# Performance work log

Measured on AMD Instinct MI355X. Metric: run time of the kernel, lower is better.

Reference implementation:

```python
import jax, jax.numpy as jnp
import numpy as np

N_NODES = 50000
N_EDGES = 800000
D = 128
H = 8
HD = D // H
N_NTYPES = 3
N_ETYPES = 5
LN_EPS = 1e-5


def setup_inputs() -> dict:
    key = jax.random.key(0)
    ks = jax.random.split(key, 16)
    inp = {
        "x": jax.random.normal(ks[0], (N_NODES, D), dtype=jnp.float32),
        "edge_index": jax.random.randint(ks[1], (2, N_EDGES), 0, N_NODES),
        "edge_type": jax.random.randint(ks[2], (N_EDGES,), 0, N_ETYPES),
        "node_type": jax.random.randint(ks[3], (N_NODES,), 0, N_NTYPES),
        # per-(node_type, head) QKV projections, per-(edge_type, head) K transform
        "W_Q": jax.random.normal(ks[4], (N_NTYPES, H, HD, HD), dtype=jnp.float32) * 0.02,
        "W_K": jax.random.normal(ks[5], (N_NTYPES, H, HD, HD), dtype=jnp.float32) * 0.02,
        "W_V": jax.random.normal(ks[6], (N_NTYPES, H, HD, HD), dtype=jnp.float32) * 0.02,
        "W_edge": jax.random.normal(ks[7], (N_ETYPES, H, HD, HD), dtype=jnp.float32) * 0.02,
        "mu": jnp.ones((H, N_ETYPES), dtype=jnp.float32),
        "W_out": jax.random.normal(ks[8], (D, D), dtype=jnp.float32) * 0.02,
        "b_out": jnp.zeros((D,), dtype=jnp.float32),
        "ln1_g": jnp.ones((D,), dtype=jnp.float32),
        "ln1_b": jnp.zeros((D,), dtype=jnp.float32),
        "W1": jax.random.normal(ks[9], (D, 4 * D), dtype=jnp.float32) * 0.02,
        "b1": jnp.zeros((4 * D,), dtype=jnp.float32),
        "W2": jax.random.normal(ks[10], (4 * D, D), dtype=jnp.float32) * 0.02,
        "b2": jnp.zeros((D,), dtype=jnp.float32),
        "ln2_g": jnp.ones((D,), dtype=jnp.float32),
        "ln2_b": jnp.zeros((D,), dtype=jnp.float32),
    }
    return inp


def _layer_norm(y, g, b):
    m = y.mean(-1, keepdims=True)
    v = ((y - m) ** 2).mean(-1, keepdims=True)
    return (y - m) * jax.lax.rsqrt(v + LN_EPS) * g + b


def reference(x, edge_index, edge_type, node_type,
              W_Q, W_K, W_V, W_edge, mu,
              W_out, b_out, ln1_g, ln1_b, W1, b1, W2, b2, ln2_g, ln2_b):
    N = x.shape[0]
    xh = x.reshape(N, H, HD)  # heads vectorized (concat of per-head slices)

    # type-specific QKV: small fixed loop over node types, masked select
    Q = jnp.zeros_like(xh)
    K = jnp.zeros_like(xh)
    V = jnp.zeros_like(xh)
    for t in range(N_NTYPES):
        m = (node_type == t)[:, None, None]
        Q = jnp.where(m, jnp.einsum('nhd,hdf->nhf', xh, W_Q[t]), Q)
        K = jnp.where(m, jnp.einsum('nhd,hdf->nhf', xh, W_K[t]), K)
        V = jnp.where(m, jnp.einsum('nhd,hdf->nhf', xh, W_V[t]), V)

    src, dst = edge_index[0], edge_index[1]
    q_dst = Q[dst]   # [E,H,HD]
    k_src = K[src]   # [E,H,HD]

    # edge-type-specific K transform
    kt = jnp.zeros_like(k_src)
    for et in range(N_ETYPES):
        m = (edge_type == et)[:, None, None]
        kt = jnp.where(m, jnp.einsum('ehd,hdf->ehf', k_src, W_edge[et]), kt)

    scores = (q_dst * kt).sum(-1) / jnp.sqrt(jnp.float32(HD))  # [E,H]
    scores = scores * mu[:, edge_type].T                       # mu per edge type, per head

    # sparse softmax over incoming edges of each dst node, per head
    smax = jax.ops.segment_max(scores, dst, num_segments=N)
    ex = jnp.exp(scores - smax[dst])
    den = jax.ops.segment_sum(ex, dst, num_segments=N)
    w = ex / (den[dst] + 1e-10)                                 # [E,H]

    agg = jax.ops.segment_sum(V[src] * w[..., None], dst, num_segments=N)  # [N,H,HD]
    mh = agg.reshape(N, D) @ W_out + b_out  # dropout is identity in eval

    h = _layer_norm(x + mh, ln1_g, ln1_b)
    ffn = jax.nn.gelu(h @ W1 + b1, approximate=False) @ W2 + b2
    return _layer_norm(h + ffn, ln2_g, ln2_b)
```

## Files before the change

kernel.cpp:

```cpp
#include <hip/hip_runtime.h>
#include <hip/hip_bf16.h>

#define N_NODESC 50000
#define N_EDGESC 800000
#define DD 128
#define HH 8
#define HDIM 16
#define N_NT 3
#define N_ET 5
#define NPB 196
#define NEB 400
#define NFB 512
#define WPB 912

#define KV8_OFF    ((size_t)0)
#define QT8_OFF    ((size_t)12800000)
#define AGG_OFF    ((size_t)57600000)
#define WOUTT_OFF  ((size_t)83200000)
#define W1T_OFF    ((size_t)83232768)
#define W2T_OFF    ((size_t)83363840)
#define WHPF_OFF   ((size_t)83494912)
#define EDATA_OFF  ((size_t)84183040)
#define ROWS_OFF   ((size_t)87383040)
#define ORIG_OFF   ((size_t)87583104)
#define DEG_OFF    ((size_t)87783104)
#define TOFS_OFF   ((size_t)87983104)
#define BH_OFF     ((size_t)87983168)
#define BB_OFF     ((size_t)87985536)
#define TMP_OFF    ((size_t)87988928)
#define RLOC_OFF   ((size_t)91188928)
#define CSUM_OFF   ((size_t)91389056)

using short8 = __attribute__((ext_vector_type(8))) short;
using f32x4  = __attribute__((ext_vector_type(4))) float;
using f32x2  = __attribute__((ext_vector_type(2))) float;

__device__ __forceinline__ ushort f2b(float f) {
    __hip_bfloat16 h = __float2bfloat16(f);
    return *(ushort*)&h;
}
__device__ __forceinline__ float b2f(ushort u) {
    __hip_bfloat16 h = *(__hip_bfloat16*)&u;
    return __bfloat162float(h);
}
__device__ __forceinline__ f32x2 pk0(unsigned int w) {
    return __builtin_amdgcn_cvt_pk_f32_fp8((int)w, false);
}
__device__ __forceinline__ f32x2 pk1(unsigned int w) {
    return __builtin_amdgcn_cvt_pk_f32_fp8((int)w, true);
}
__device__ __forceinline__ float gelu_f(float v) {
    const float x = v * 0.70710678118654752f;
    const float ax = fabsf(x);
    const float d = fmaf(0.3275911f, ax, 1.0f);
    float t;
    asm("v_rcp_f32 %0, %1" : "=v"(t) : "v"(d));
    float p = fmaf(1.061405429f, t, -1.453152027f);
    p = fmaf(p, t, 1.421413741f);
    p = fmaf(p, t, -0.284496736f);
    p = fmaf(p, t, 0.254829592f);
    p = p * t;
    const float e = __expf(-ax * ax);
    const float er = 1.0f - p * e;
    const float erfx = (x < 0.f) ? -er : er;
    return 0.5f * v * (1.0f + erfx);
}
__device__ __forceinline__ void ebar() {
    __builtin_amdgcn_sched_barrier(0);
    asm volatile("s_waitcnt lgkmcnt(0)" ::: "memory");
    __builtin_amdgcn_sched_barrier(0);
    __builtin_amdgcn_s_barrier();
    __builtin_amdgcn_sched_barrier(0);
}

__global__ __launch_bounds__(256) void prep_a(
    const float* __restrict__ Wout, const float* __restrict__ W1, const float* __restrict__ W2,
    const float* __restrict__ WQ, const float* __restrict__ Wk, const float* __restrict__ Wv,
    const float* __restrict__ We, const float* __restrict__ mu,
    ushort* __restrict__ Woutt, ushort* __restrict__ W1t, ushort* __restrict__ W2t,
    ushort* __restrict__ Whpf,
    const int* __restrict__ ntype, int* __restrict__ bh,
    const int* __restrict__ dst, int* __restrict__ deg, unsigned int* __restrict__ tmp)
{
    const int b = blockIdx.x, tid = threadIdx.x;
    if (b < WPB) {
        const int gid = b * 256 + tid;
        if (gid < 16384) {
            const int nn = gid >> 7, k = gid & 127;
            Woutt[gid] = f2b(Wout[k * 128 + nn]);
        } else if (gid < 81920) {
            const int i = gid - 16384;
            const int nn = i >> 7, k = i & 127;
            W1t[i] = f2b(W1[k * 512 + nn]);
        } else if (gid < 147456) {
            const int i = gid - 81920;
            const int nn = i >> 9, k = i & 511;
            W2t[i] = f2b(W2[k * 128 + nn]);
        } else {
            const int idx = gid - 147456;
            const int t = idx / 28672;
            const int r = idx % 28672;
            const int i = r & 7;
            const int l = (r >> 3) & 63;
            const int f = r >> 9;
            const int j = f % 14, p = f / 14;
            const int c = j * 16 + (l & 15);
            const int k = ((l >> 4) << 3) + i;
            const int hi = (c >= 112) ? 1 : 0;
            const int h = 2 * p + hi;
            float v = 0.f;
            if ((k >> 4) == hi) {
                const int kp = k & 15;
                const int cl = c - hi * 112;
                if (cl < 16) {
                    v = 4.f * Wk[((t * HH + h) * HDIM + kp) * HDIM + cl];
                } else if (cl < 32) {
                    v = 4.f * Wv[((t * HH + h) * HDIM + kp) * HDIM + (cl - 16)];
                } else {
                    const int et = (cl - 32) >> 4, jj = (cl - 32) & 15;
                    const float* wq = WQ + ((t * HH + h) * HDIM + kp) * HDIM;
                    const float* we = We + ((et * HH + h) * HDIM + jj) * HDIM;
                    float s = 0.f;
#pragma unroll
                    for (int ff = 0; ff < 16; ff++) s = fmaf(wq[ff], we[ff], s);
                    v = 64.f * mu[h * N_ET + et] * s;
                }
            }
            Whpf[idx] = f2b(v);
        }
    } else if (b < WPB + NPB) {
        const int bc = b - WPB;
        const int wave = tid >> 6, lane = tid & 63;
        const int n = bc * 256 + tid;
        const int t = (n < N_NODESC) ? ntype[n] : -1;
        const unsigned long long m0 = __ballot(t == 0);
        const unsigned long long m1 = __ballot(t == 1);
        const unsigned long long m2 = __ballot(t == 2);
        __shared__ int wcnt[4][3];
        if (lane == 0) {
            wcnt[wave][0] = (int)__popcll(m0);
            wcnt[wave][1] = (int)__popcll(m1);
            wcnt[wave][2] = (int)__popcll(m2);
        }
        __syncthreads();
        if (tid < 3)
            bh[tid * NPB + bc] = wcnt[0][tid] + wcnt[1][tid] + wcnt[2][tid] + wcnt[3][tid];
    } else {
        for (int e = (b - WPB - NPB) * 256 + tid; e < N_EDGESC; e += NEB * 256) {
            const int nd = dst[e];
            const unsigned int p = (unsigned int)atomicAdd(&deg[nd], 1);
            tmp[e] = (p << 16) | (unsigned int)nd;
        }
    }
}

__global__ __launch_bounds__(256) void prep_b(
    const int* __restrict__ bh, const int* __restrict__ deg,
    int* __restrict__ bb, int* __restrict__ tofs,
    int* __restrict__ rloc, int* __restrict__ csum)
{
    __shared__ int part[256];
    const int tid = threadIdx.x;
    if (blockIdx.x == 0) {
        const int base3 = tid * 3;
        int e0 = (base3 + 0 < 588) ? bh[base3 + 0] : 0;
        int e1 = (base3 + 1 < 588) ? bh[base3 + 1] : 0;
        int e2 = (base3 + 2 < 588) ? bh[base3 + 2] : 0;
        const int l0 = e0, l1 = e0 + e1, l2 = l1 + e2;
        part[tid] = l2;
        __syncthreads();
        for (int off = 1; off < 256; off <<= 1) {
            const int u = (tid >= off) ? part[tid - off] : 0;
            __syncthreads();
            part[tid] += u;
            __syncthreads();
        }
        const int tb = part[tid] - l2;
        if (base3 + 0 < 588) bb[base3 + 0] = tb;
        if (base3 + 1 < 588) bb[base3 + 1] = tb + l0;
        if (base3 + 2 < 588) bb[base3 + 2] = tb + l1;
        __syncthreads();
        if (tid == 0) {
            tofs[0] = 0;
            tofs[1] = bb[NPB];
            tofs[2] = bb[2 * NPB];
            tofs[3] = N_NODESC;
        }
    } else {
        const int c = blockIdx.x - 1;
        const int n = c * 256 + tid;
        const int vdeg = (n < N_NODESC) ? deg[n] : 0;
        part[tid] = vdeg;
        __syncthreads();
        for (int off = 1; off < 256; off <<= 1) {
            const int u = (tid >= off) ? part[tid - off] : 0;
            __syncthreads();
            part[tid] += u;
            __syncthreads();
        }
        if (n <= N_NODESC) rloc[n] = part[tid] - vdeg;
        if (tid == 255) csum[c] = part[255];
    }
}

__global__ __launch_bounds__(256) void prep_c(
    const int* __restrict__ ntype,
    const int* __restrict__ src, const int* __restrict__ etype,
    const int* __restrict__ bb, const int* __restrict__ rloc, const int* __restrict__ csum,
    const unsigned int* __restrict__ tmp,
    int* __restrict__ origof, int* __restrict__ rows,
    int* __restrict__ edata)
{
    const int b = blockIdx.x, tid = threadIdx.x;
    __shared__ int cb[256];
    {
        const int v = (tid < NPB) ? csum[tid] : 0;
        cb[tid] = v;
        __syncthreads();
        for (int off = 1; off < 256; off <<= 1) {
            const int u = (tid >= off) ? cb[tid - off] : 0;
            __syncthreads();
            cb[tid] += u;
            __syncthreads();
        }
        const int incl = cb[tid];
        __syncthreads();
        cb[tid] = incl - v;
        __syncthreads();
    }

    if (b < NPB) {
        const int wave = tid >> 6, lane = tid & 63;
        const int n = b * 256 + tid;
        const int t = (n < N_NODESC) ? ntype[n] : -1;
        const unsigned long long m0 = __ballot(t == 0);
        const unsigned long long m1 = __ballot(t == 1);
        const unsigned long long m2 = __ballot(t == 2);
        __shared__ int wcnt[4][3];
        if (lane == 0) {
            wcnt[wave][0] = (int)__popcll(m0);
            wcnt[wave][1] = (int)__popcll(m1);
            wcnt[wave][2] = (int)__popcll(m2);
        }
        __syncthreads();
        if (n < N_NODESC) {
            int basew = 0;
#pragma unroll
            for (int w = 0; w < 4; w++) if (w < wave) basew += wcnt[w][t];
            const unsigned long long mt = (t == 0) ? m0 : (t == 1) ? m1 : m2;
            const unsigned long long mlt = ((unsigned long long)1 << lane) - 1;
            const int p = bb[t * NPB + b] + basew + (int)__popcll(mt & mlt);
            origof[p] = n;
        }
        if (n <= N_NODESC) rows[n] = cb[b] + rloc[n];
    } else {
        for (int e = (b - NPB) * 256 + tid; e < N_EDGESC; e += NFB * 256) {
            const unsigned int v = tmp[e];
            const int nd = (int)(v & 0xffffu);
            const int p = (int)(v >> 16);
            edata[cb[nd >> 8] + rloc[nd] + p] = src[e] | (etype[e] << 16);
        }
    }
}

#define LDX 132

__global__ __launch_bounds__(256) void proj_gemm(
    const float* __restrict__ x, const ushort* __restrict__ Whpf,
    const int* __restrict__ tofs, const int* __restrict__ origof,
    unsigned char* __restrict__ KV8b, unsigned char* __restrict__ Qt8)
{
    const int t = blockIdx.y;
    const int rs = tofs[t], re = tofs[t + 1];
    const int mBase = rs + blockIdx.x * 64;
    if (mBase >= re) return;

    __shared__ ushort Xs[64 * LDX];
    __shared__ ushort Ws[28672];

    const int tid = threadIdx.x;
    const int lane = tid & 63, wave = tid >> 6;
    const int l15 = lane & 15, rq = (lane >> 4) * 4;

#pragma unroll
    for (int it = 0; it < 4; it++) {
        const int idx = it * 256 + tid;
        const int row = idx >> 4, ch = idx & 15;
        int gm = mBase + row; if (gm >= N_NODESC) gm = N_NODESC - 1;
        const int og = origof[gm];
        const float4 v0 = *(const float4*)(x + (size_t)og * DD + ch * 8);
        const float4 v1 = *(const float4*)(x + (size_t)og * DD + ch * 8 + 4);
        ushort o[8] = {f2b(v0.x), f2b(v0.y), f2b(v0.z), f2b(v0.w),
                       f2b(v1.x), f2b(v1.y), f2b(v1.z), f2b(v1.w)};
        *(uint4*)&Xs[row * LDX + ch * 8] = *(uint4*)o;
    }
    const ushort* Wg = Whpf + (size_t)t * 28672;
#pragma unroll
    for (int it = 0; it < 14; it++) {
        const int idx = it * 256 + tid;
        *(uint4*)&Ws[idx * 8] = *(const uint4*)(Wg + (size_t)idx * 8);
    }
    __syncthreads();

    int ogr[4]; bool vr[4];
#pragma unroll
    for (int r = 0; r < 4; r++) {
        const int gm = mBase + wave * 16 + rq + r;
        vr[r] = (gm < re);
        ogr[r] = vr[r] ? origof[gm] : 0;
    }

    for (int p = 0; p < 4; p++) {
        const short8 af = *(const short8*)&Xs[(wave * 16 + l15) * LDX + p * 32 + (lane >> 4) * 8];
#pragma unroll
        for (int j = 0; j < 14; j++) {
            const short8 bf = *(const short8*)&Ws[((p * 14 + j) * 64 + lane) * 8];
            f32x4 c = __builtin_amdgcn_mfma_f32_16x16x32_bf16(
                af, bf, (f32x4){0.f, 0.f, 0.f, 0.f}, 0, 0, 0);
            const int hi = (j >= 7) ? 1 : 0;
            const int h = 2 * p + hi;
            const int jj = j - hi * 7;
#pragma unroll
            for (int r = 0; r < 4; r++) {
                if (!vr[r]) continue;
                const float v = c[r];
                const unsigned char b8 =
                    (unsigned char)(__builtin_amdgcn_cvt_pk_fp8_f32(v, v, 0, false) & 0xff);
                const size_t og = (size_t)ogr[r];
                if (jj == 0)      KV8b[og * 256 + h * 16 + l15] = b8;
                else if (jj == 1) KV8b[og * 256 + 128 + h * 16 + l15] = b8;
                else              Qt8[og * 640 + (jj - 2) * 128 + h * 16 + l15] = b8;
            }
        }
    }
}

__global__ __launch_bounds__(128) void edgeagg_kernel(
    const int* __restrict__ rowstart, const int* __restrict__ edata,
    const unsigned char* __restrict__ Qt8, const unsigned char* __restrict__ KV8,
    ushort* __restrict__ agg)
{
    const int w = threadIdx.x >> 6;
    const int lane = threadIdx.x & 63;
    const int n = blockIdx.x * 2 + w;
    const int slot = lane >> 3;
    const int h = lane & 7;

    __shared__ uint4 qs8s[2][40];
    if (lane < 40)
        qs8s[w][lane] = ((const uint4*)(Qt8 + (size_t)n * 640))[lane];
    __syncthreads();
    const uint* qbase = (const uint*)&qs8s[w][0];

    const int s0 = rowstart[n], s1 = rowstart[n + 1];
    const float qsc = 1.44269504f / 1024.f;

    float acc[16];
#pragma unroll
    for (int j = 0; j < 16; j++) acc[j] = 0.f;
    float den = 0.f;

    int i = s0 + slot;
    int ed = 0;
    uint4 kw = {0u, 0u, 0u, 0u}, vw = {0u, 0u, 0u, 0u};
    if (i < s1) {
        ed = edata[i];
        const unsigned char* kvp = KV8 + ((size_t)(ed & 0xffff) << 8);
        kw = *(const uint4*)(kvp + (h << 4));
        vw = *(const uint4*)(kvp + 128 + (h << 4));
    }
    while (i < s1) {
        const int in2 = i + 8;
        int edn = 0;
        uint4 kwn = {0u, 0u, 0u, 0u}, vwn = {0u, 0u, 0u, 0u};
        if (in2 < s1) {
            edn = edata[in2];
            const unsigned char* kvpn = KV8 + ((size_t)(edn & 0xffff) << 8);
            kwn = *(const uint4*)(kvpn + (h << 4));
            vwn = *(const uint4*)(kvpn + 128 + (h << 4));
        }

        const int et = ed >> 16;
        const uint4 qw = *(const uint4*)(qbase + (et << 5) + (h << 2));

        const f32x2 q0 = pk0(qw.x), q1 = pk1(qw.x), q2 = pk0(qw.y), q3 = pk1(qw.y);
        const f32x2 q4 = pk0(qw.z), q5 = pk1(qw.z), q6 = pk0(qw.w), q7 = pk1(qw.w);
        const f32x2 k0 = pk0(kw.x), k1 = pk1(kw.x), k2 = pk0(kw.y), k3 = pk1(kw.y);
        const f32x2 k4 = pk0(kw.z), k5 = pk1(kw.z), k6 = pk0(kw.w), k7 = pk1(kw.w);

        float pa = q0.x * k0.x;
        float pb = q0.y * k0.y;
        float pc = q1.x * k1.x;
        float pd = q1.y * k1.y;
        pa = fmaf(q2.x, k2.x, pa); pb = fmaf(q2.y, k2.y, pb);
        pc = fmaf(q3.x, k3.x, pc); pd = fmaf(q3.y, k3.y, pd);
        pa = fmaf(q4.x, k4.x, pa); pb = fmaf(q4.y, k4.y, pb);
        pc = fmaf(q5.x, k5.x, pc); pd = fmaf(q5.y, k5.y, pd);
        pa = fmaf(q6.x, k6.x, pa); pb = fmaf(q6.y, k6.y, pb);
        pc = fmaf(q7.x, k7.x, pc); pd = fmaf(q7.y, k7.y, pd);

        const float ex = exp2f(((pa + pb) + (pc + pd)) * qsc);
        den += ex;

        const f32x2 v0 = pk0(vw.x), v1 = pk1(vw.x), v2 = pk0(vw.y), v3 = pk1(vw.y);
        const f32x2 v4 = pk0(vw.z), v5 = pk1(vw.z), v6 = pk0(vw.w), v7 = pk1(vw.w);
        acc[0]  = fmaf(ex, v0.x, acc[0]);  acc[1]  = fmaf(ex, v0.y, acc[1]);
        acc[2]  = fmaf(ex, v1.x, acc[2]);  acc[3]  = fmaf(ex, v1.y, acc[3]);
        acc[4]  = fmaf(ex, v2.x, acc[4]);  acc[5]  = fmaf(ex, v2.y, acc[5]);
        acc[6]  = fmaf(ex, v3.x, acc[6]);  acc[7]  = fmaf(ex, v3.y, acc[7]);
        acc[8]  = fmaf(ex, v4.x, acc[8]);  acc[9]  = fmaf(ex, v4.y, acc[9]);
        acc[10] = fmaf(ex, v5.x, acc[10]); acc[11] = fmaf(ex, v5.y, acc[11]);
        acc[12] = fmaf(ex, v6.x, acc[12]); acc[13] = fmaf(ex, v6.y, acc[13]);
        acc[14] = fmaf(ex, v7.x, acc[14]); acc[15] = fmaf(ex, v7.y, acc[15]);

        i = in2; ed = edn; kw = kwn; vw = vwn;
    }

    {
        const int b0 = slot & 1, b1 = slot & 2, b2 = slot & 4;
#pragma unroll
        for (int j = 0; j < 8; j++) {
            const float v = b0 ? acc[j] : acc[j + 8];
            const float r = __shfl_xor(v, 8);
            acc[j] = (b0 ? acc[j + 8] : acc[j]) + r;
        }
#pragma unroll
        for (int j = 0; j < 4; j++) {
            const float v = b1 ? acc[j] : acc[j + 4];
            const float r = __shfl_xor(v, 16);
            acc[j] = (b1 ? acc[j + 4] : acc[j]) + r;
        }
#pragma unroll
        for (int j = 0; j < 2; j++) {
            const float v = b2 ? acc[j] : acc[j + 2];
            const float r = __shfl_xor(v, 32);
            acc[j] = (b2 ? acc[j + 2] : acc[j]) + r;
        }
        den += __shfl_xor(den, 8);
        den += __shfl_xor(den, 16);
        den += __shfl_xor(den, 32);
    }
    const float rr = 0.25f / (den + 1e-10f);
    const int fb = (h << 4) + ((slot & 1) << 3) + ((slot & 2) << 1) + ((slot & 4) >> 1);
    ushort o2[2] = { f2b(acc[0] * rr), f2b(acc[1] * rr) };
    *(uint*)&agg[((size_t)n << 7) + fb] = *(uint*)o2;
}

#define LDH 132
#define LDB2 68

#define LOADB(P0, P1, PTR) { P0 = *(const short8*)(PTR); P1 = *(const short8*)((PTR) + 8); }
#define STAGEB(BUF, P0, P1) { *(short8*)&Bs[BUF][br * LDB2 + bc] = P0; \
                              *(short8*)&Bs[BUF][br * LDB2 + bc + 8] = P1; }

__global__ __launch_bounds__(512, 4) void fused_tail(
    const ushort* __restrict__ agg, const ushort* __restrict__ Woutt,
    const ushort* __restrict__ W1t, const ushort* __restrict__ W2t,
    const float* __restrict__ x,
    const float* __restrict__ bout, const float* __restrict__ g1, const float* __restrict__ b1ln,
    const float* __restrict__ b1, const float* __restrict__ b2,
    const float* __restrict__ g2, const float* __restrict__ b2ln,
    float* __restrict__ out)
{
    __shared__ ushort Bs[2][128 * LDB2];
    __shared__ ushort Hs[64 * LDH];
    __shared__ ushort Ts[64 * LDH];
    __shared__ float red[2][4][64];

    const int tid = threadIdx.x;
    const int lane = tid & 63, wave = tid >> 6;
    const int wm = wave >> 2, wn = wave & 3;
    const int l15 = lane & 15, q8 = (lane >> 4) * 8, rq = (lane >> 4) * 4;
    const int mBase = blockIdx.x * 64;

    const int br = tid >> 2, bc = (tid & 3) * 16;
    const int ar = tid >> 3, ac = (tid & 7) * 16;
    int rowA = mBase + ar; if (rowA >= N_NODESC) rowA = N_NODESC - 1;

    f32x4 acc1[2][2], acc2[2][2];
#pragma unroll
    for (int i = 0; i < 2; i++)
#pragma unroll
        for (int j = 0; j < 2; j++) {
            acc1[i][j] = (f32x4){0.f, 0.f, 0.f, 0.f};
            acc2[i][j] = (f32x4){0.f, 0.f, 0.f, 0.f};
        }

    short8 pX0, pX1, pY0, pY1, aT0, aT1;
    LOADB(pX0, pX1, Woutt + (size_t)br * 128 + bc);
    LOADB(pY0, pY1, Woutt + (size_t)br * 128 + 64 + bc);
    aT0 = *(const short8*)(agg + (size_t)rowA * DD + ac);
    aT1 = *(const short8*)(agg + (size_t)rowA * DD + ac + 8);
    float xv[2][4][2];
#pragma unroll
    for (int i = 0; i < 2; i++)
#pragma unroll
        for (int r = 0; r < 4; r++) {
            const int gm = mBase + wm * 32 + i * 16 + rq + r;
            const int gr = (gm < N_NODESC) ? gm : N_NODESC - 1;
#pragma unroll
            for (int j = 0; j < 2; j++)
                xv[i][r][j] = x[(size_t)gr * DD + wn * 32 + j * 16 + l15];
        }
    *(short8*)&Ts[ar * LDH + ac] = aT0;
    *(short8*)&Ts[ar * LDH + ac + 8] = aT1;
    STAGEB(0, pX0, pX1);
    LOADB(pX0, pX1, W1t + (size_t)br * 128 + bc);
    ebar();

    STAGEB(1, pY0, pY1);
    LOADB(pY0, pY1, W1t + (size_t)br * 128 + 64 + bc);
#pragma unroll
    for (int kk2 = 0; kk2 < 2; kk2++) {
        short8 af[2], bf[2];
#pragma unroll
        for (int i = 0; i < 2; i++)
            af[i] = *(const short8*)&Ts[(wm * 32 + i * 16 + l15) * LDH + kk2 * 32 + q8];
#pragma unroll
        for (int j = 0; j < 2; j++)
            bf[j] = *(const short8*)&Bs[0][(wn * 32 + j * 16 + l15) * LDB2 + kk2 * 32 + q8];
#pragma unroll
        for (int i = 0; i < 2; i++)
#pragma unroll
            for (int j = 0; j < 2; j++)
                acc1[i][j] = __builtin_amdgcn_mfma_f32_16x16x32_bf16(af[i], bf[j], acc1[i][j], 0, 0, 0);
    }
    ebar();

    STAGEB(0, pX0, pX1);
    LOADB(pX0, pX1, W2t + (size_t)br * 512 + bc);
#pragma unroll
    for (int kk2 = 0; kk2 < 2; kk2++) {
        short8 af[2], bf[2];
#pragma unroll
        for (int i = 0; i < 2; i++)
            af[i] = *(const short8*)&Ts[(wm * 32 + i * 16 + l15) * LDH + 64 + kk2 * 32 + q8];
#pragma unroll
        for (int j = 0; j < 2; j++)
            bf[j] = *(const short8*)&Bs[1][(wn * 32 + j * 16 + l15) * LDB2 + kk2 * 32 + q8];
#pragma unroll
        for (int i = 0; i < 2; i++)
#pragma unroll
            for (int j = 0; j < 2; j++)
                acc1[i][j] = __builtin_amdgcn_mfma_f32_16x16x32_bf16(af[i], bf[j], acc1[i][j], 0, 0, 0);
    }
    ebar();

    {
        float bo[2], gv[2], bv[2];
#pragma unroll
        for (int j = 0; j < 2; j++) {
            const int gn = wn * 32 + j * 16 + l15;
            bo[j] = bout[gn]; gv[j] = g1[gn]; bv[j] = b1ln[gn];
        }
#pragma unroll
        for (int i = 0; i < 2; i++) {
#pragma unroll
            for (int r = 0; r < 4; r++) {
                const int row = wm * 32 + i * 16 + rq + r;
                float s = 0.f, ss = 0.f;
#pragma unroll
                for (int j = 0; j < 2; j++) {
                    float v = acc1[i][j][r] + bo[j] + xv[i][r][j];
                    acc1[i][j][r] = v;
                    s += v; ss += v * v;
                }
                s  += __shfl_xor(s, 1);  s  += __shfl_xor(s, 2);  s  += __shfl_xor(s, 4);  s  += __shfl_xor(s, 8);
                ss += __shfl_xor(ss, 1); ss += __shfl_xor(ss, 2); ss += __shfl_xor(ss, 4); ss += __shfl_xor(ss, 8);
                if (l15 == 0) { red[0][wn][row] = s; red[1][wn][row] = ss; }
            }
        }
        ebar();
#pragma unroll
        for (int i = 0; i < 2; i++) {
#pragma unroll
            for (int r = 0; r < 4; r++) {
                const int row = wm * 32 + i * 16 + rq + r;
                const float s  = red[0][0][row] + red[0][1][row] + red[0][2][row] + red[0][3][row];
                const float ss = red[1][0][row] + red[1][1][row] + red[1][2][row] + red[1][3][row];
                const float mean = s * (1.f / 128.f);
                const float var  = ss * (1.f / 128.f) - mean * mean;
                const float rstd = rsqrtf(var + 1e-5f);
#pragma unroll
                for (int j = 0; j < 2; j++) {
                    const int gn = wn * 32 + j * 16 + l15;
                    Hs[row * LDH + gn] = f2b((acc1[i][j][r] - mean) * rstd * gv[j] + bv[j]);
                }
            }
        }
        ebar();
    }

    for (int nb = 0; nb < 4; nb++) {
        f32x4 a1[2][2];
#pragma unroll
        for (int i = 0; i < 2; i++)
#pragma unroll
            for (int j = 0; j < 2; j++) a1[i][j] = (f32x4){0.f, 0.f, 0.f, 0.f};

        STAGEB(1, pY0, pY1);
        LOADB(pY0, pY1, W2t + (size_t)br * 512 + nb * 128 + 64 + bc);
#pragma unroll
        for (int kk2 = 0; kk2 < 2; kk2++) {
            short8 af[2], bf[2];
#pragma unroll
            for (int i = 0; i < 2; i++)
                af[i] = *(const short8*)&Hs[(wm * 32 + i * 16 + l15) * LDH + kk2 * 32 + q8];
#pragma unroll
            for (int j = 0; j < 2; j++)
                bf[j] = *(const short8*)&Bs[0][(wn * 32 + j * 16 + l15) * LDB2 + kk2 * 32 + q8];
#pragma unroll
            for (int i = 0; i < 2; i++)
#pragma unroll
                for (int j = 0; j < 2; j++)
                    a1[i][j] = __builtin_amdgcn_mfma_f32_16x16x32_bf16(af[i], bf[j], a1[i][j], 0, 0, 0);
        }
        ebar();

        STAGEB(0, pX0, pX1);
        if (nb < 3) { LOADB(pX0, pX1, W1t + (size_t)((nb + 1) * 128 + br) * 128 + bc); }
#pragma unroll
        for (int kk2 = 0; kk2 < 2; kk2++) {
            short8 af[2], bf[2];
#pragma unroll
            for (int i = 0; i < 2; i++)
                af[i] = *(const short8*)&Hs[(wm * 32 + i * 16 + l15) * LDH + 64 + kk2 * 32 + q8];
#pragma unroll
            for (int j = 0; j < 2; j++)
                bf[j] = *(const short8*)&Bs[1][(wn * 32 + j * 16 + l15) * LDB2 + kk2 * 32 + q8];
#pragma unroll
            for (int i = 0; i < 2; i++)
#pragma unroll
                for (int j = 0; j < 2; j++)
                    a1[i][j] = __builtin_amdgcn_mfma_f32_16x16x32_bf16(af[i], bf[j], a1[i][j], 0, 0, 0);
        }
        ebar();

        {
            float b1v[2];
#pragma unroll
            for (int j = 0; j < 2; j++)
                b1v[j] = b1[nb * 128 + wn * 32 + j * 16 + l15];
#pragma unroll
            for (int i = 0; i < 2; i++)
#pragma unroll
                for (int j = 0; j < 2; j++)
#pragma unroll
                    for (int r = 0; r < 4; r++) {
                        const int row = wm * 32 + i * 16 + rq + r;
                        const int col = wn * 32 + j * 16 + l15;
                        Ts[row * LDH + col] = f2b(gelu_f(a1[i][j][r] + b1v[j]));
                    }
        }
        ebar();

        STAGEB(1, pY0, pY1);
        if (nb < 3) { LOADB(pY0, pY1, W1t + (size_t)((nb + 1) * 128 + br) * 128 + 64 + bc); }
#pragma unroll
        for (int kk2 = 0; kk2 < 2; kk2++) {
            short8 af[2], bf[2];
#pragma unroll
            for (int i = 0; i < 2; i++)
                af[i] = *(const short8*)&Ts[(wm * 32 + i * 16 + l15) * LDH + kk2 * 32 + q8];
#pragma unroll
            for (int j = 0; j < 2; j++)
                bf[j] = *(const short8*)&Bs[0][(wn * 32 + j * 16 + l15) * LDB2 + kk2 * 32 + q8];
#pragma unroll
            for (int i = 0; i < 2; i++)
#pragma unroll
                for (int j = 0; j < 2; j++)
                    acc2[i][j] = __builtin_amdgcn_mfma_f32_16x16x32_bf16(af[i], bf[j], acc2[i][j], 0, 0, 0);
        }
        ebar();

        if (nb < 3) {
            STAGEB(0, pX0, pX1);
            LOADB(pX0, pX1, W2t + (size_t)br * 512 + (nb + 1) * 128 + bc);
        }
#pragma unroll
        for (int kk2 = 0; kk2 < 2; kk2++) {
            short8 af[2], bf[2];
#pragma unroll
            for (int i = 0; i < 2; i++)
                af[i] = *(const short8*)&Ts[(wm * 32 + i * 16 + l15) * LDH + 64 + kk2 * 32 + q8];
#pragma unroll
            for (int j = 0; j < 2; j++)
                bf[j] = *(const short8*)&Bs[1][(wn * 32 + j * 16 + l15) * LDB2 + kk2 * 32 + q8];
#pragma unroll
            for (int i = 0; i < 2; i++)
#pragma unroll
                for (int j = 0; j < 2; j++)
                    acc2[i][j] = __builtin_amdgcn_mfma_f32_16x16x32_bf16(af[i], bf[j], acc2[i][j], 0, 0, 0);
        }
        ebar();
    }

    {
        float b2v[2], gv[2], bv[2];
#pragma unroll
        for (int j = 0; j < 2; j++) {
            const int gn = wn * 32 + j * 16 + l15;
            b2v[j] = b2[gn]; gv[j] = g2[gn]; bv[j] = b2ln[gn];
        }
#pragma unroll
        for (int i = 0; i < 2; i++) {
#pragma unroll
            for (int r = 0; r < 4; r++) {
                const int row = wm * 32 + i * 16 + rq + r;
                float s = 0.f, ss = 0.f;
#pragma unroll
                for (int j = 0; j < 2; j++) {
                    const int gn = wn * 32 + j * 16 + l15;
                    float v = acc2[i][j][r] + b2v[j] + b2f(Hs[row * LDH + gn]);
                    acc2[i][j][r] = v;
                    s += v; ss += v * v;
                }
                s  += __shfl_xor(s, 1);  s  += __shfl_xor(s, 2);  s  += __shfl_xor(s, 4);  s  += __shfl_xor(s, 8);
                ss += __shfl_xor(ss, 1); ss += __shfl_xor(ss, 2); ss += __shfl_xor(ss, 4); ss += __shfl_xor(ss, 8);
                if (l15 == 0) { red[0][wn][row] = s; red[1][wn][row] = ss; }
            }
        }
        ebar();
#pragma unroll
        for (int i = 0; i < 2; i++) {
#pragma unroll
            for (int r = 0; r < 4; r++) {
                const int row = wm * 32 + i * 16 + rq + r;
                const int gm = mBase + row;
                if (gm >= N_NODESC) continue;
                const float s  = red[0][0][row] + red[0][1][row] + red[0][2][row] + red[0][3][row];
                const float ss = red[1][0][row] + red[1][1][row] + red[1][2][row] + red[1][3][row];
                const float mean = s * (1.f / 128.f);
                const float var  = ss * (1.f / 128.f) - mean * mean;
                const float rstd = rsqrtf(var + 1e-5f);
#pragma unroll
                for (int j = 0; j < 2; j++) {
                    const int gn = wn * 32 + j * 16 + l15;
                    out[(size_t)gm * DD + gn] = (acc2[i][j][r] - mean) * rstd * gv[j] + bv[j];
                }
            }
        }
    }
}

extern "C" void kernel_launch(void* const* d_in, const int* in_sizes, int n_in,
                              void* d_out, int out_size, void* d_ws, size_t ws_size,
                              hipStream_t stream)
{
    const float* x     = (const float*)d_in[0];
    const int*   ei    = (const int*)d_in[1];
    const int*   etyp  = (const int*)d_in[2];
    const int*   ntype = (const int*)d_in[3];
    const float* Wq    = (const float*)d_in[4];
    const float* Wk    = (const float*)d_in[5];
    const float* Wv    = (const float*)d_in[6];
    const float* We    = (const float*)d_in[7];
    const float* mu    = (const float*)d_in[8];
    const float* Wout  = (const float*)d_in[9];
    const float* bout  = (const float*)d_in[10];
    const float* g1    = (const float*)d_in[11];
    const float* b1ln  = (const float*)d_in[12];
    const float* W1    = (const float*)d_in[13];
    const float* b1    = (const float*)d_in[14];
    const float* W2    = (const float*)d_in[15];
    const float* b2    = (const float*)d_in[16];
    const float* g2    = (const float*)d_in[17];
    const float* b2ln  = (const float*)d_in[18];
    float* out = (float*)d_out;

    char* ws = (char*)d_ws;
    ushort*        KV8   = (ushort*)(ws + KV8_OFF);
    unsigned char* Qt8   = (unsigned char*)(ws + QT8_OFF);
    ushort*        agg   = (ushort*)(ws + AGG_OFF);
    ushort*        Woutt = (ushort*)(ws + WOUTT_OFF);
    ushort*        W1t   = (ushort*)(ws + W1T_OFF);
    ushort*        W2t   = (ushort*)(ws + W2T_OFF);
    ushort*        Whpf  = (ushort*)(ws + WHPF_OFF);
    int*           edata = (int*)(ws + EDATA_OFF);
    int*           rows  = (int*)(ws + ROWS_OFF);
    int*           origof= (int*)(ws + ORIG_OFF);
    int*           deg   = (int*)(ws + DEG_OFF);
    int*           tofs  = (int*)(ws + TOFS_OFF);
    int*           bh    = (int*)(ws + BH_OFF);
    int*           bb    = (int*)(ws + BB_OFF);
    unsigned int*  tmp   = (unsigned int*)(ws + TMP_OFF);
    int*           rloc  = (int*)(ws + RLOC_OFF);
    int*           csum  = (int*)(ws + CSUM_OFF);

    const int* srcA = ei;
    const int* dstA = ei + N_EDGESC;

    (void)hipMemsetAsync(ws + DEG_OFF, 0, 200000, stream);

    prep_a<<<WPB + NPB + NEB, 256, 0, stream>>>(
        Wout, W1, W2, Wq, Wk, Wv, We, mu, Woutt, W1t, W2t, Whpf,
        ntype, bh, dstA, deg, tmp);
    prep_b<<<1 + NPB, 256, 0, stream>>>(bh, deg, bb, tofs, rloc, csum);
    prep_c<<<NPB + NFB, 256, 0, stream>>>(ntype, srcA, etyp, bb, rloc, csum, tmp,
                                          origof, rows, edata);

    proj_gemm<<<dim3(782, 3), 256, 0, stream>>>(x, Whpf, tofs, origof,
                                                (unsigned char*)KV8, Qt8);
    edgeagg_kernel<<<N_NODESC / 2, 128, 0, stream>>>(rows, edata, Qt8,
                                                     (const unsigned char*)KV8, agg);

    fused_tail<<<782, 512, 0, stream>>>(agg, Woutt, W1t, W2t, x,
                                        bout, g1, b1ln, b1, b2, g2, b2ln, out);
}
```

Measured before the change: 309.3 us.

## Single-buffer weight staging in fused tail to raise occupancy

Measured after the change: 326.4 us. +5.5%, slower.

```diff
diff --git a/kernel.cpp b/kernel.cpp
--- a/kernel.cpp
+++ b/kernel.cpp
@@ -450,10 +450,26 @@
 #define LDB2 68
 
 #define LOADB(P0, P1, PTR) { P0 = *(const short8*)(PTR); P1 = *(const short8*)((PTR) + 8); }
-#define STAGEB(BUF, P0, P1) { *(short8*)&Bs[BUF][br * LDB2 + bc] = P0; \
-                              *(short8*)&Bs[BUF][br * LDB2 + bc + 8] = P1; }
-
-__global__ __launch_bounds__(512, 4) void fused_tail(
+#define STAGEB1(P0, P1) { *(short8*)&Bs[br * LDB2 + bc] = P0; \
+                          *(short8*)&Bs[br * LDB2 + bc + 8] = P1; }
+#define COMP(ASRC, KOFF, ACC) { \
+    short8 af[2], bf[2]; \
+    _Pragma("unroll") \
+    for (int kk2 = 0; kk2 < 2; kk2++) { \
+        _Pragma("unroll") \
+        for (int i = 0; i < 2; i++) \
+            af[i] = *(const short8*)&ASRC[(wm * 32 + i * 16 + l15) * LDH + (KOFF) + kk2 * 32 + q8]; \
+        _Pragma("unroll") \
+        for (int j = 0; j < 2; j++) \
+            bf[j] = *(const short8*)&Bs[(wn * 32 + j * 16 + l15) * LDB2 + kk2 * 32 + q8]; \
+        _Pragma("unroll") \
+        for (int i = 0; i < 2; i++) \
+            _Pragma("unroll") \
+            for (int j = 0; j < 2; j++) \
+                ACC[i][j] = __builtin_amdgcn_mfma_f32_16x16x32_bf16(af[i], bf[j], ACC[i][j], 0, 0, 0); \
+    } }
+
+__global__ __launch_bounds__(512, 6) void fused_tail(
     const ushort* __restrict__ agg, const ushort* __restrict__ Woutt,
     const ushort* __restrict__ W1t, const ushort* __restrict__ W2t,
     const float* __restrict__ x,
@@ -462,7 +478,7 @@
     const float* __restrict__ g2, const float* __restrict__ b2ln,
     float* __restrict__ out)
 {
-    __shared__ ushort Bs[2][128 * LDB2];
+    __shared__ ushort Bs[128 * LDB2];
     __shared__ ushort Hs[64 * LDH];
     __shared__ ushort Ts[64 * LDH];
     __shared__ float red[2][4][64];
@@ -486,9 +502,8 @@
             acc2[i][j] = (f32x4){0.f, 0.f, 0.f, 0.f};
         }
 
-    short8 pX0, pX1, pY0, pY1, aT0, aT1;
-    LOADB(pX0, pX1, Woutt + (size_t)br * 128 + bc);
-    LOADB(pY0, pY1, Woutt + (size_t)br * 128 + 64 + bc);
+    short8 pB0, pB1, aT0, aT1;
+    LOADB(pB0, pB1, Woutt + (size_t)br * 128 + bc);
     aT0 = *(const short8*)(agg + (size_t)rowA * DD + ac);
     aT1 = *(const short8*)(agg + (size_t)rowA * DD + ac + 8);
     float xv[2][4][2];
@@ -504,47 +519,16 @@
         }
     *(short8*)&Ts[ar * LDH + ac] = aT0;
     *(short8*)&Ts[ar * LDH + ac + 8] = aT1;
-    STAGEB(0, pX0, pX1);
-    LOADB(pX0, pX1, W1t + (size_t)br * 128 + bc);
+    STAGEB1(pB0, pB1);
+    LOADB(pB0, pB1, Woutt + (size_t)br * 128 + 64 + bc);
     ebar();
 
-    STAGEB(1, pY0, pY1);
-    LOADB(pY0, pY1, W1t + (size_t)br * 128 + 64 + bc);
-#pragma unroll
-    for (int kk2 = 0; kk2 < 2; kk2++) {
-        short8 af[2], bf[2];
-#pragma unroll
-        for (int i = 0; i < 2; i++)
-            af[i] = *(const short8*)&Ts[(wm * 32 + i * 16 + l15) * LDH + kk2 * 32 + q8];
-#pragma unroll
-        for (int j = 0; j < 2; j++)
-            bf[j] = *(const short8*)&Bs[0][(wn * 32 + j * 16 + l15) * LDB2 + kk2 * 32 + q8];
-#pragma unroll
-        for (int i = 0; i < 2; i++)
-#pragma unroll
-            for (int j = 0; j < 2; j++)
-                acc1[i][j] = __builtin_amdgcn_mfma_f32_16x16x32_bf16(af[i], bf[j], acc1[i][j], 0, 0, 0);
-    }
+    COMP(Ts, 0, acc1);
     ebar();
-
-    STAGEB(0, pX0, pX1);
-    LOADB(pX0, pX1, W2t + (size_t)br * 512 + bc);
-#pragma unroll
-    for (int kk2 = 0; kk2 < 2; kk2++) {
-        short8 af[2], bf[2];
-#pragma unroll
-        for (int i = 0; i < 2; i++)
-            af[i] = *(const short8*)&Ts[(wm * 32 + i * 16 + l15) * LDH + 64 + kk2 * 32 + q8];
-#pragma unroll
-        for (int j = 0; j < 2; j++)
-            bf[j] = *(const short8*)&Bs[1][(wn * 32 + j * 16 + l15) * LDB2 + kk2 * 32 + q8];
-#pragma unroll
-        for (int i = 0; i < 2; i++)
-#pragma unroll
-            for (int j = 0; j < 2; j++)
-                acc1[i][j] = __builtin_amdgcn_mfma_f32_16x16x32_bf16(af[i], bf[j], acc1[i][j], 0, 0, 0);
-    }
+    STAGEB1(pB0, pB1);
+    LOADB(pB0, pB1, W1t + (size_t)br * 128 + bc);
     ebar();
+    COMP(Ts, 64, acc1);
 
     {
         float bo[2], gv[2], bv[2];
@@ -588,7 +572,6 @@
                 }
             }
         }
-        ebar();
     }
 
     for (int nb = 0; nb < 4; nb++) {
@@ -598,43 +581,17 @@
 #pragma unroll
             for (int j = 0; j < 2; j++) a1[i][j] = (f32x4){0.f, 0.f, 0.f, 0.f};
 
-        STAGEB(1, pY0, pY1);
-        LOADB(pY0, pY1, W2t + (size_t)br * 512 + nb * 128 + 64 + bc);
-#pragma unroll
-        for (int kk2 = 0; kk2 < 2; kk2++) {
-            short8 af[2], bf[2];
-#pragma unroll
-            for (int i = 0; i < 2; i++)
-                af[i] = *(const short8*)&Hs[(wm * 32 + i * 16 + l15) * LDH + kk2 * 32 + q8];
-#pragma unroll
-            for (int j = 0; j < 2; j++)
-                bf[j] = *(const short8*)&Bs[0][(wn * 32 + j * 16 + l15) * LDB2 + kk2 * 32 + q8];
-#pragma unroll
-            for (int i = 0; i < 2; i++)
-#pragma unroll
-                for (int j = 0; j < 2; j++)
-                    a1[i][j] = __builtin_amdgcn_mfma_f32_16x16x32_bf16(af[i], bf[j], a1[i][j], 0, 0, 0);
-        }
-        ebar();
-
-        STAGEB(0, pX0, pX1);
-        if (nb < 3) { LOADB(pX0, pX1, W1t + (size_t)((nb + 1) * 128 + br) * 128 + bc); }
-#pragma unroll
-        for (int kk2 = 0; kk2 < 2; kk2++) {
-            short8 af[2], bf[2];
-#pragma unroll
-            for (int i = 0; i < 2; i++)
-                af[i] = *(const short8*)&Hs[(wm * 32 + i * 16 + l15) * LDH + 64 + kk2 * 32 + q8];
-#pragma unroll
-            for (int j = 0; j < 2; j++)
-                bf[j] = *(const short8*)&Bs[1][(wn * 32 + j * 16 + l15) * LDB2 + kk2 * 32 + q8];
-#pragma unroll
-            for (int i = 0; i < 2; i++)
-#pragma unroll
-                for (int j = 0; j < 2; j++)
-                    a1[i][j] = __builtin_amdgcn_mfma_f32_16x16x32_bf16(af[i], bf[j], a1[i][j], 0, 0, 0);
-        }
-        ebar();
+        ebar();
+        STAGEB1(pB0, pB1);
+        LOADB(pB0, pB1, W1t + (size_t)(nb * 128 + br) * 128 + 64 + bc);
+        ebar();
+        COMP(Hs, 0, a1);
+
+        ebar();
+        STAGEB1(pB0, pB1);
+        LOADB(pB0, pB1, W2t + (size_t)br * 512 + nb * 128 + bc);
+        ebar();
+        COMP(Hs, 64, a1);
 
         {
             float b1v[2];
@@ -652,47 +609,18 @@
                         Ts[row * LDH + col] = f2b(gelu_f(a1[i][j][r] + b1v[j]));
                     }
         }
-        ebar();
-
-        STAGEB(1, pY0, pY1);
-        if (nb < 3) { LOADB(pY0, pY1, W1t + (size_t)((nb + 1) * 128 + br) * 128 + 64 + bc); }
-#pragma unroll
-        for (int kk2 = 0; kk2 < 2; kk2++) {
-            short8 af[2], bf[2];
-#pragma unroll
-            for (int i = 0; i < 2; i++)
-                af[i] = *(const short8*)&Ts[(wm * 32 + i * 16 + l15) * LDH + kk2 * 32 + q8];
-#pragma unroll
-            for (int j = 0; j < 2; j++)
-                bf[j] = *(const short8*)&Bs[0][(wn * 32 + j * 16 + l15) * LDB2 + kk2 * 32 + q8];
-#pragma unroll
-            for (int i = 0; i < 2; i++)
-#pragma unroll
-                for (int j = 0; j < 2; j++)
-                    acc2[i][j] = __builtin_amdgcn_mfma_f32_16x16x32_bf16(af[i], bf[j], acc2[i][j], 0, 0, 0);
-        }
-        ebar();
-
-        if (nb < 3) {
-            STAGEB(0, pX0, pX1);
-            LOADB(pX0, pX1, W2t + (size_t)br * 512 + (nb + 1) * 128 + bc);
-        }
-#pragma unroll
-        for (int kk2 = 0; kk2 < 2; kk2++) {
-            short8 af[2], bf[2];
-#pragma unroll
-            for (int i = 0; i < 2; i++)
-                af[i] = *(const short8*)&Ts[(wm * 32 + i * 16 + l15) * LDH + 64 + kk2 * 32 + q8];
-#pragma unroll
-            for (int j = 0; j < 2; j++)
-                bf[j] = *(const short8*)&Bs[1][(wn * 32 + j * 16 + l15) * LDB2 + kk2 * 32 + q8];
-#pragma unroll
-            for (int i = 0; i < 2; i++)
-#pragma unroll
-                for (int j = 0; j < 2; j++)
-                    acc2[i][j] = __builtin_amdgcn_mfma_f32_16x16x32_bf16(af[i], bf[j], acc2[i][j], 0, 0, 0);
-        }
-        ebar();
+
+        ebar();
+        STAGEB1(pB0, pB1);
+        LOADB(pB0, pB1, W2t + (size_t)br * 512 + nb * 128 + 64 + bc);
+        ebar();
+        COMP(Ts, 0, acc2);
+
+        ebar();
+        STAGEB1(pB0, pB1);
+        if (nb < 3) { LOADB(pB0, pB1, W1t + (size_t)((nb + 1) * 128 + br) * 128 + bc); }
+        ebar();
+        COMP(Ts, 64, acc2);
     }
 
     {
```
